# Performance work log

Hardware: AMD Instinct MI355X
Metric: run time of the kernel (lower is better)

## Reference

```python
import jax, jax.numpy as jnp
import numpy as np

N_LEVELS = 256  # 2**8

def setup_inputs() -> dict:
    key = jax.random.key(0)
    k1, k2, k3, k4 = jax.random.split(key, 4)
    x = jax.random.normal(k1, (4, 4096, 4096), dtype=jnp.float32)
    # medians increase across MAD iterations (inliers are zeroed each round)
    medians = jnp.sort(jax.random.uniform(k2, (10,), dtype=jnp.float32, minval=0.5, maxval=4.0))
    deltas = jax.random.uniform(k3, (10,), dtype=jnp.float32, minval=0.005, maxval=0.05)
    zero_points = jnp.round(jax.random.uniform(k4, (10,), dtype=jnp.float32) * (N_LEVELS - 1))
    return {"x": x, "medians": medians, "deltas": deltas, "zero_points": zero_points}

def reference(x, medians, deltas, zero_points):
    G = medians.shape[0]  # number of MAD groups (== max_iters kept)
    x_abs = jnp.abs(x)
    # group id = number of medians <= |x|, clamped — same as the torch loop of comparisons
    grp = jnp.zeros(x.shape, dtype=jnp.int32)
    for i in range(G):  # G is small and static (10)
        grp = grp + (x_abs >= medians[i]).astype(jnp.int32)
    grp = jnp.clip(grp, 0, G - 1)
    d = deltas[grp]
    zp = zero_points[grp]
    x_quant = jnp.clip(jnp.round(x / d) + zp, 0.0, N_LEVELS - 1)
    return (x_quant - zp) * d
```

## Files before the change

### kernel.cpp

```cpp
#include <hip/hip_runtime.h>

#define G 10

typedef float f32x4 __attribute__((ext_vector_type(4)));

__global__ __launch_bounds__(256, 8) void madq_kernel(
    const float* __restrict__ x,
    const float* __restrict__ medians,
    const float* __restrict__ deltas,
    const float* __restrict__ zps,
    float* __restrict__ out,
    int n4)
{
    float m[G - 1];
#pragma unroll
    for (int i = 0; i < G - 1; ++i) m[i] = medians[i];

    const int lane = threadIdx.x & 63;
    float d_l = 1.0f, zp_l = 0.0f;
    if (lane < G) { d_l = deltas[lane]; zp_l = zps[lane]; }
    float r_l = __builtin_amdgcn_rcpf(d_l);
    r_l = fmaf(fmaf(-d_l, r_l, 1.0f), r_l, r_l);

    auto proc = [&](f32x4 v) -> f32x4 {
        f32x4 o;
#pragma unroll
        for (int e = 0; e < 4; ++e) {
            float xv = v[e];
            float xa = fabsf(xv);
            int ib = 0;
#pragma unroll
            for (int i = 1; i < G; ++i)
                ib = (xa >= m[i - 1]) ? (4 * i) : ib;
            float d  = __int_as_float(__builtin_amdgcn_ds_bpermute(ib, __float_as_int(d_l)));
            float r  = __int_as_float(__builtin_amdgcn_ds_bpermute(ib, __float_as_int(r_l)));
            float zp = __int_as_float(__builtin_amdgcn_ds_bpermute(ib, __float_as_int(zp_l)));
            float q0 = xv * r;
            float t  = fmaf(fmaf(-d, q0, xv), r, q0);
            t = rintf(t);
            float hi = 255.0f - zp;
            t = __builtin_amdgcn_fmed3f(t, -zp, hi);
            o[e] = t * d;
        }
        return o;
    };

    const f32x4* __restrict__ x4 = (const f32x4*)x;
    f32x4* __restrict__ o4 = (f32x4*)out;
    const int stride = gridDim.x * blockDim.x;
    int i = blockIdx.x * blockDim.x + threadIdx.x;

    for (; i + 3 * stride < n4; i += 4 * stride) {
        f32x4 v0 = __builtin_nontemporal_load(&x4[i]);
        f32x4 v1 = __builtin_nontemporal_load(&x4[i + stride]);
        f32x4 v2 = __builtin_nontemporal_load(&x4[i + 2 * stride]);
        f32x4 v3 = __builtin_nontemporal_load(&x4[i + 3 * stride]);
        f32x4 r0 = proc(v0);
        f32x4 r1 = proc(v1);
        f32x4 r2 = proc(v2);
        f32x4 r3 = proc(v3);
        __builtin_nontemporal_store(r0, &o4[i]);
        __builtin_nontemporal_store(r1, &o4[i + stride]);
        __builtin_nontemporal_store(r2, &o4[i + 2 * stride]);
        __builtin_nontemporal_store(r3, &o4[i + 3 * stride]);
    }
    for (; i < n4; i += stride) {
        f32x4 v = __builtin_nontemporal_load(&x4[i]);
        __builtin_nontemporal_store(proc(v), &o4[i]);
    }
}

extern "C" void kernel_launch(void* const* d_in, const int* in_sizes, int n_in,
                              void* d_out, int out_size, void* d_ws, size_t ws_size,
                              hipStream_t stream) {
    const float* x       = (const float*)d_in[0];
    const float* medians = (const float*)d_in[1];
    const float* deltas  = (const float*)d_in[2];
    const float* zps     = (const float*)d_in[3];
    float*       out     = (float*)d_out;

    int n  = in_sizes[0];
    int n4 = n / 4;
    const int block = 256;
    long long want = ((long long)n4 + block * 4 - 1) / (block * 4);
    int grid = (int)(want < 1 ? 1 : (want > 2048 ? 2048 : want));
    madq_kernel<<<grid, block, 0, stream>>>(x, medians, deltas, zps, out, n4);
}
```

Measured before the change: 440.5 us.

## Software-pipeline chunked loads with register double-buffering per block

Each block now processes contiguous 16 KB chunks and loads the next chunk's four vectors into registers before computing and storing the current chunk, so memory latency overlaps with compute. The per-block access pattern changes from a grid-strided interleave to contiguous chunks, and the launch-bounds occupancy hint drops from 8 to 6 waves to leave room for the extra live registers. Block 0 handles the tail. Lower occupancy and higher register pressure may cancel some of the latency hiding in this memory-bound kernel.

```diff
diff --git a/kernel.cpp b/kernel.cpp
--- a/kernel.cpp
+++ b/kernel.cpp
@@ -1,10 +1,11 @@
 #include <hip/hip_runtime.h>
 
 #define G 10
+#define CH 1024
 
 typedef float f32x4 __attribute__((ext_vector_type(4)));
 
-__global__ __launch_bounds__(256, 8) void madq_kernel(
+__global__ __launch_bounds__(256, 6) void madq_kernel(
     const float* __restrict__ x,
     const float* __restrict__ medians,
     const float* __restrict__ deltas,
@@ -36,37 +37,54 @@
             float r  = __int_as_float(__builtin_amdgcn_ds_bpermute(ib, __float_as_int(r_l)));
             float zp = __int_as_float(__builtin_amdgcn_ds_bpermute(ib, __float_as_int(zp_l)));
             float q0 = xv * r;
-            float t  = fmaf(fmaf(-d, q0, xv), r, q0);
-            t = rintf(t);
-            float hi = 255.0f - zp;
-            t = __builtin_amdgcn_fmed3f(t, -zp, hi);
-            o[e] = t * d;
+            float t2 = fmaf(fmaf(-d, q0, xv), r, q0);
+            t2 = rintf(t2);
+            t2 = __builtin_amdgcn_fmed3f(t2, -zp, 255.0f - zp);
+            o[e] = t2 * d;
         }
         return o;
     };
 
     const f32x4* __restrict__ x4 = (const f32x4*)x;
     f32x4* __restrict__ o4 = (f32x4*)out;
-    const int stride = gridDim.x * blockDim.x;
-    int i = blockIdx.x * blockDim.x + threadIdx.x;
+    const int t = threadIdx.x;
+    const int nch = n4 / CH;
+    const int step = gridDim.x;
 
-    for (; i + 3 * stride < n4; i += 4 * stride) {
-        f32x4 v0 = __builtin_nontemporal_load(&x4[i]);
-        f32x4 v1 = __builtin_nontemporal_load(&x4[i + stride]);
-        f32x4 v2 = __builtin_nontemporal_load(&x4[i + 2 * stride]);
-        f32x4 v3 = __builtin_nontemporal_load(&x4[i + 3 * stride]);
-        f32x4 r0 = proc(v0);
-        f32x4 r1 = proc(v1);
-        f32x4 r2 = proc(v2);
-        f32x4 r3 = proc(v3);
-        __builtin_nontemporal_store(r0, &o4[i]);
-        __builtin_nontemporal_store(r1, &o4[i + stride]);
-        __builtin_nontemporal_store(r2, &o4[i + 2 * stride]);
-        __builtin_nontemporal_store(r3, &o4[i + 3 * stride]);
+    int c = blockIdx.x;
+    f32x4 a0, a1, a2, a3;
+    if (c < nch) {
+        const f32x4* p = x4 + c * CH + t;
+        a0 = __builtin_nontemporal_load(p);
+        a1 = __builtin_nontemporal_load(p + 256);
+        a2 = __builtin_nontemporal_load(p + 512);
+        a3 = __builtin_nontemporal_load(p + 768);
     }
-    for (; i < n4; i += stride) {
-        f32x4 v = __builtin_nontemporal_load(&x4[i]);
-        __builtin_nontemporal_store(proc(v), &o4[i]);
+    while (c < nch) {
+        const int cn = c + step;
+        f32x4 b0, b1, b2, b3;
+        const bool have = cn < nch;
+        if (have) {
+            const f32x4* p = x4 + cn * CH + t;
+            b0 = __builtin_nontemporal_load(p);
+            b1 = __builtin_nontemporal_load(p + 256);
+            b2 = __builtin_nontemporal_load(p + 512);
+            b3 = __builtin_nontemporal_load(p + 768);
+        }
+        f32x4* q = o4 + c * CH + t;
+        __builtin_nontemporal_store(proc(a0), q);
+        __builtin_nontemporal_store(proc(a1), q + 256);
+        __builtin_nontemporal_store(proc(a2), q + 512);
+        __builtin_nontemporal_store(proc(a3), q + 768);
+        if (have) { a0 = b0; a1 = b1; a2 = b2; a3 = b3; }
+        c = cn;
+    }
+
+    if (blockIdx.x == 0) {
+        for (int i = nch * CH + t; i < n4; i += 256) {
+            f32x4 v = __builtin_nontemporal_load(&x4[i]);
+            __builtin_nontemporal_store(proc(v), &o4[i]);
+        }
     }
 }
 
@@ -81,8 +99,7 @@
 
     int n  = in_sizes[0];
     int n4 = n / 4;
-    const int block = 256;
-    long long want = ((long long)n4 + block * 4 - 1) / (block * 4);
-    int grid = (int)(want < 1 ? 1 : (want > 2048 ? 2048 : want));
-    madq_kernel<<<grid, block, 0, stream>>>(x, medians, deltas, zps, out, n4);
+    int nch = n4 / CH;
+    int grid = nch < 1 ? 1 : (nch > 2048 ? 2048 : nch);
+    madq_kernel<<<grid, 256, 0, stream>>>(x, medians, deltas, zps, out, n4);
 }
```

After: 424.3 us. -3.7%, faster.
